# Performance work log

Hardware: AMD Instinct MI355X
Metric: run time of the kernel (lower is better)

Reference implementation:

```python
import jax, jax.numpy as jnp
import numpy as np

B, S, D, H, W = 4, 2048, 512, 8, 16
DK = D // H


def setup_inputs() -> dict:
    key = jax.random.key(0)
    ks = jax.random.split(key, 11)
    scale = 1.0 / np.sqrt(D)
    return {
        "query": jax.random.normal(ks[0], (B, S, D), jnp.float32),
        "key": jax.random.normal(ks[1], (B, S, D), jnp.float32),
        "value": jax.random.normal(ks[2], (B, S, D), jnp.float32),
        "Wq": jax.random.normal(ks[3], (D, D), jnp.float32) * scale,
        "bq": jnp.zeros((D,), jnp.float32),
        "Wk": jax.random.normal(ks[4], (D, D), jnp.float32) * scale,
        "bk": jnp.zeros((D,), jnp.float32),
        "Wv": jax.random.normal(ks[5], (D, D), jnp.float32) * scale,
        "bv": jnp.zeros((D,), jnp.float32),
        "Wo": jax.random.normal(ks[6], (D, D), jnp.float32) * scale,
        "bo": jnp.zeros((D,), jnp.float32),
    }


def reference(query, key, value, Wq, bq, Wk, bk, Wv, bv, Wo, bo):
    b, s, d = query.shape
    # QKV projections -> [b, H, s, DK]
    Q = (query @ Wq + bq).reshape(b, s, H, DK).transpose(0, 2, 1, 3)
    K = (key @ Wk + bk).reshape(b, s, H, DK).transpose(0, 2, 1, 3)
    V = (value @ Wv + bv).reshape(b, s, H, DK).transpose(0, 2, 1, 3)
    # Dense scores (faithful to original O(n^2) math), then static band mask
    scores = jnp.einsum("bhqd,bhkd->bhqk", Q, K) / jnp.sqrt(jnp.array(DK, scores_dtype := Q.dtype))
    idx = jnp.arange(s)
    local = jnp.abs(idx[:, None] - idx[None, :]) <= W  # [s, s] band
    mask_value = jnp.finfo(scores.dtype).min
    scores = jnp.where(local[None, None], scores, mask_value)
    attn = jax.nn.softmax(scores, axis=-1)
    ctx = jnp.einsum("bhqk,bhkd->bhqd", attn, V)
    ctx = ctx.transpose(0, 2, 1, 3).reshape(b, s, d)
    return ctx @ Wo + bo
```

## Files before the change

### kernel.cpp

```cpp
#include <hip/hip_runtime.h>

typedef __attribute__((ext_vector_type(8))) short bf16x8;
typedef __attribute__((ext_vector_type(4))) float f32x4;
typedef __attribute__((ext_vector_type(4))) unsigned int u32x4;
typedef __attribute__((ext_vector_type(8))) unsigned short bfu8;

#define BB 4
#define SS 2048
#define DD 512
#define HH 8
#define DKK 64
#define WWIN 16
#define MTOT (BB*SS)
#define MKE  ((long)MTOT*DD)
#define NKE  ((long)DD*DD)

__device__ __forceinline__ unsigned short f2bf(float f) {
  unsigned int u = __float_as_uint(f);
  u += 0x7fffu + ((u >> 16) & 1u);
  return (unsigned short)(u >> 16);
}
__device__ __forceinline__ float bf2f(unsigned short s) {
  return __uint_as_float(((unsigned int)s) << 16);
}

__device__ __forceinline__ void gload_lds16(const unsigned short* g, unsigned short* l) {
  __builtin_amdgcn_global_load_lds((const __attribute__((address_space(1))) void*)g,
                                   (__attribute__((address_space(3))) void*)l, 16, 0, 0);
}

__global__ __launch_bounds__(256) void convert_w(
    const float* __restrict__ Wq, const float* __restrict__ Wk,
    const float* __restrict__ Wv, const float* __restrict__ Wo,
    const float* __restrict__ bq, const float* __restrict__ bk, const float* __restrict__ bv,
    unsigned short* __restrict__ wt, float* __restrict__ bias_all)
{
  int bx = blockIdx.x;
  if (bx >= 256) {
    int idx = (bx - 256) * 256 + threadIdx.x;
    bias_all[idx] = idx < DD ? bq[idx] : (idx < 2*DD ? bk[idx-DD] : bv[idx-2*DD]);
    return;
  }
  int wm = bx >> 6;
  int tile = bx & 63;
  int tr = tile >> 3, tc = tile & 7;
  const float* src = wm==0 ? Wq : wm==1 ? Wk : wm==2 ? Wv : Wo;
  unsigned short* dst = wt + (long)wm*NKE;
  __shared__ float tl[64][65];
  int t = threadIdx.x;
  int cr = t >> 6;
  int cc = t & 63;
  for (int p = 0; p < 16; ++p) {
    int row = p*4 + cr;
    tl[row][cc] = src[(long)(tr*64+row)*DD + tc*64 + cc];
  }
  __syncthreads();
  for (int p = 0; p < 16; ++p) {
    int orow = p*4 + cr;
    dst[(long)(tc*64 + orow)*DD + tr*64 + cc] = f2bf(tl[cc][orow]);
  }
}

template<int OUT_BF16, int A_FP32>
__global__ __launch_bounds__(256, 2) void gemm_dbuf(
    const void* __restrict__ a0, const void* __restrict__ a1, const void* __restrict__ a2,
    const unsigned short* __restrict__ Btbase, long bZ,
    const float* __restrict__ biasBase, long biasZ,
    void* __restrict__ outBase, long outZ, int N, int K)
{
  const int bid   = blockIdx.x;
  const int slot  = bid >> 3;
  const int panel = (bid & 7) + 8 * (slot >> 2);
  const int n0 = (slot & 3) * 128;
  const int z  = panel >> 6;
  const int m0 = (panel & 63) * 128;

  const void* Av = z==0 ? a0 : z==1 ? a1 : a2;
  const unsigned short* Bt = Btbase + (long)z*bZ;
  const float* bias = biasBase + (long)z*biasZ;

  const int tid = threadIdx.x, lane = tid & 63, w = tid >> 6;
  const int wr = w >> 1, wc = w & 1;
  const int c = lane & 15, g = lane >> 4;

  __shared__ unsigned short lA[2][128*64];
  __shared__ unsigned short lB[2][128*64];

  f32x4 acc[4][4] = {};
  float4 fa[8];
  const int NT = K >> 6;

  auto stageB = [&](int buf, int kt) {
    #pragma unroll
    for (int j = 0; j < 4; ++j) {
      int u = w*256 + j*64 + lane;
      int row = u >> 3, sl = (u & 7) ^ (row & 7);
      gload_lds16(Bt + (long)(n0 + row)*K + kt + sl*8, &lB[buf][(w*256 + j*64)*8]);
    }
  };
  auto stageA_lds = [&](int buf, int kt) {
    const unsigned short* Ab = (const unsigned short*)Av;
    #pragma unroll
    for (int j = 0; j < 4; ++j) {
      int u = w*256 + j*64 + lane;
      int row = u >> 3, sl = (u & 7) ^ (row & 7);
      gload_lds16(Ab + (long)(m0 + row)*K + kt + sl*8, &lA[buf][(w*256 + j*64)*8]);
    }
  };
  auto loadA = [&](int kt) {
    const float* Af = (const float*)Av;
    #pragma unroll
    for (int i = 0; i < 4; ++i) {
      int u = i*256 + tid;
      int row = u >> 3, col = (u & 7) * 8;
      const float* s = Af + (long)(m0 + row)*K + kt + col;
      fa[2*i]   = *(const float4*)s;
      fa[2*i+1] = *(const float4*)(s + 4);
    }
  };
  auto writeA = [&](int buf) {
    #pragma unroll
    for (int i = 0; i < 4; ++i) {
      int u = i*256 + tid;
      int row = u >> 3, sl = u & 7;
      bfu8 o;
      o[0]=f2bf(fa[2*i].x);   o[1]=f2bf(fa[2*i].y);   o[2]=f2bf(fa[2*i].z);   o[3]=f2bf(fa[2*i].w);
      o[4]=f2bf(fa[2*i+1].x); o[5]=f2bf(fa[2*i+1].y); o[6]=f2bf(fa[2*i+1].z); o[7]=f2bf(fa[2*i+1].w);
      *(bfu8*)&lA[buf][row*64 + (sl ^ (row & 7))*8] = o;
    }
  };
  auto compute = [&](int buf) {
    #pragma unroll
    for (int kk = 0; kk < 2; ++kk) {
      bf16x8 af[4], bfr[4];
      #pragma unroll
      for (int m = 0; m < 4; ++m) {
        int row = wr*64 + m*16 + c;
        af[m] = *reinterpret_cast<const bf16x8*>(&lA[buf][row*64 + (((kk<<2)+g) ^ (row & 7))*8]);
      }
      #pragma unroll
      for (int nn = 0; nn < 4; ++nn) {
        int col = wc*64 + nn*16 + c;
        bfr[nn] = *reinterpret_cast<const bf16x8*>(&lB[buf][col*64 + (((kk<<2)+g) ^ (col & 7))*8]);
      }
      __builtin_amdgcn_s_setprio(1);
      #pragma unroll
      for (int m = 0; m < 4; ++m)
        #pragma unroll
        for (int nn = 0; nn < 4; ++nn)
          acc[m][nn] = __builtin_amdgcn_mfma_f32_16x16x32_bf16(af[m], bfr[nn], acc[m][nn], 0, 0, 0);
      __builtin_amdgcn_s_setprio(0);
    }
  };

  if (A_FP32) loadA(0); else stageA_lds(0, 0);
  stageB(0, 0);
  if (A_FP32) writeA(0);
  __syncthreads();

  int cur = 0;
  for (int t = 0; t < NT; ++t) {
    int nxt = cur ^ 1;
    if (t + 1 < NT) {
      if (A_FP32) loadA((t+1) << 6); else stageA_lds(nxt, (t+1) << 6);
      stageB(nxt, (t+1) << 6);
    }
    compute(cur);
    if (A_FP32 && t + 1 < NT) writeA(nxt);
    __syncthreads();
    cur = nxt;
  }

  #pragma unroll
  for (int m = 0; m < 4; ++m) {
    int rbase = m0 + wr*64 + m*16 + g*4;
    #pragma unroll
    for (int nn = 0; nn < 4; ++nn) {
      int col = n0 + wc*64 + nn*16 + c;
      float bv = bias[col];
      #pragma unroll
      for (int r = 0; r < 4; ++r) {
        float val = acc[m][nn][r] + bv;
        long idx = (long)z*outZ + (long)(rbase + r)*N + col;
        if (OUT_BF16) ((unsigned short*)outBase)[idx] = f2bf(val);
        else          ((float*)outBase)[idx] = val;
      }
    }
  }
}

#define KP 76
#define PP 76
__global__ __launch_bounds__(256) void attn_kernel(
    const unsigned short* __restrict__ Qbf, const unsigned short* __restrict__ Kbf,
    const unsigned short* __restrict__ Vbf, unsigned short* __restrict__ ctxbf)
{
  const int q0 = blockIdx.x * 128;
  const int h  = blockIdx.y;
  const int b  = blockIdx.z;
  const int tid = threadIdx.x, lane = tid & 63, w = tid >> 6;
  const int c = lane & 15, g = lane >> 4;
  const int w0 = q0 - WWIN;

  __shared__ unsigned short K_l[160*KP];
  __shared__ unsigned short V_l[160*KP];
  __shared__ unsigned short P_l[4][32*PP];

  const long baseRow = (long)b*SS*DD + (long)h*DKK;
  const int qw0   = q0 + w*32;
  const int kbase = w*32;

  bf16x8 aq[2][2];
  for (int m = 0; m < 2; ++m)
    for (int kk = 0; kk < 2; ++kk)
      aq[m][kk] = *reinterpret_cast<const bf16x8*>(
          Qbf + baseRow + (long)(qw0 + m*16 + c)*DD + kk*32 + g*8);

  for (int i = 0; i < 5; ++i) {
    int u = i*256 + tid;
    int row = u >> 3, c8 = (u & 7) * 8;
    int gk = w0 + row;
    u32x4 kv = {0,0,0,0}, vv = {0,0,0,0};
    if (gk >= 0 && gk < SS) {
      kv = *(const u32x4*)(Kbf + baseRow + (long)gk*DD + c8);
      vv = *(const u32x4*)(Vbf + baseRow + (long)gk*DD + c8);
    }
    *(u32x4*)(&K_l[row*KP + c8]) = kv;
    *(u32x4*)(&V_l[row*KP + c8]) = vv;
  }
  __syncthreads();

  f32x4 accs[2][4] = {};
  __builtin_amdgcn_s_setprio(1);
  for (int kk = 0; kk < 2; ++kk) {
    bf16x8 bk[4];
    for (int n = 0; n < 4; ++n)
      bk[n] = *reinterpret_cast<const bf16x8*>(&K_l[(kbase + n*16 + c)*KP + kk*32 + g*8]);
    for (int m = 0; m < 2; ++m)
      for (int n = 0; n < 4; ++n)
        accs[m][n] = __builtin_amdgcn_mfma_f32_16x16x32_bf16(aq[m][kk], bk[n], accs[m][n], 0, 0, 0);
  }
  __builtin_amdgcn_s_setprio(0);

  float pden[2][4];
  for (int m = 0; m < 2; ++m) {
    for (int r = 0; r < 4; ++r) {
      int qi = m*16 + g*4 + r;
      float sv[4];
      float mx = -INFINITY;
      for (int n = 0; n < 4; ++n) {
        int kr = n*16 + c;
        int d  = kr - qi;
        int kg = w0 + kbase + kr;
        bool ok = (d >= 0) && (d <= 2*WWIN) && (kg >= 0) && (kg < SS);
        sv[n] = ok ? accs[m][n][r] * 0.125f : -INFINITY;
        mx = fmaxf(mx, sv[n]);
      }
      for (int off = 1; off < 16; off <<= 1) mx = fmaxf(mx, __shfl_xor(mx, off, 64));
      float sum = 0.f;
      for (int n = 0; n < 4; ++n) {
        float e = __expf(sv[n] - mx);
        sum += e;
        P_l[w][(m*16 + g*4 + r)*PP + n*16 + c] = f2bf(e);
      }
      for (int off = 1; off < 16; off <<= 1) sum += __shfl_xor(sum, off, 64);
      pden[m][r] = sum;
    }
  }
  __syncthreads();

  f32x4 acco[2][4] = {};
  for (int kk = 0; kk < 2; ++kk) {
    bf16x8 pa[2];
    for (int m = 0; m < 2; ++m)
      pa[m] = *reinterpret_cast<const bf16x8*>(&P_l[w][(m*16 + c)*PP + kk*32 + g*8]);
    bf16x8 bv[4];
    int kb = kbase + kk*32 + g*8;
    for (int n = 0; n < 4; ++n) {
      bfu8 t;
      for (int j = 0; j < 8; ++j) t[j] = V_l[(kb + j)*KP + n*16 + c];
      bv[n] = *reinterpret_cast<bf16x8*>(&t);
    }
    __builtin_amdgcn_s_setprio(1);
    for (int m = 0; m < 2; ++m)
      for (int n = 0; n < 4; ++n)
        acco[m][n] = __builtin_amdgcn_mfma_f32_16x16x32_bf16(pa[m], bv[n], acco[m][n], 0, 0, 0);
    __builtin_amdgcn_s_setprio(0);
  }

  for (int m = 0; m < 2; ++m) {
    for (int r = 0; r < 4; ++r) {
      int q = qw0 + m*16 + g*4 + r;
      float inv = 1.f / pden[m][r];
      for (int n = 0; n < 4; ++n)
        ctxbf[baseRow + (long)q*DD + n*16 + c] = f2bf(acco[m][n][r] * inv);
    }
  }
}

extern "C" void kernel_launch(void* const* d_in, const int* in_sizes, int n_in,
                              void* d_out, int out_size, void* d_ws, size_t ws_size,
                              hipStream_t stream) {
  const float* q  = (const float*)d_in[0];
  const float* k  = (const float*)d_in[1];
  const float* v  = (const float*)d_in[2];
  const float* Wq = (const float*)d_in[3];
  const float* bq = (const float*)d_in[4];
  const float* Wk = (const float*)d_in[5];
  const float* bk = (const float*)d_in[6];
  const float* Wv = (const float*)d_in[7];
  const float* bv = (const float*)d_in[8];
  const float* Wo = (const float*)d_in[9];
  const float* bo = (const float*)d_in[10];

  char* ws = (char*)d_ws;
  unsigned short* wtbf     = (unsigned short*)(ws);
  float*          bias_all = (float*)(ws + 2097152);
  unsigned short* qkvbf    = (unsigned short*)(ws + 2103296);
  unsigned short* ctxbf    = (unsigned short*)(ws + 27269120);

  convert_w<<<262, 256, 0, stream>>>(Wq, Wk, Wv, Wo, bq, bk, bv, wtbf, bias_all);
  gemm_dbuf<1,1><<<768, 256, 0, stream>>>(
      q, k, v, wtbf, NKE, bias_all, DD,
      (void*)qkvbf, MKE, DD, DD);
  attn_kernel<<<dim3(SS/128, HH, BB), 256, 0, stream>>>(
      qkvbf, qkvbf + MKE, qkvbf + 2*MKE, ctxbf);
  gemm_dbuf<0,0><<<256, 256, 0, stream>>>(
      ctxbf, ctxbf, ctxbf, wtbf + 3*NKE, 0, bo, 0,
      (void*)d_out, 0, DD, DD);
}
```

Before: 158.4 us.

## Replace LDS double buffering with register-staged single-buffer GEMM pipeline

The GEMM kernel drops direct global-to-LDS loads and double-buffered shared memory. It now prefetches the next A and B tiles into registers while computing on a single LDS buffer, then writes them to LDS between explicit barriers. Halving LDS use allows raising the occupancy hint from 2 to 3 blocks per CU. The cost is two barriers per iteration and more register pressure, and the bf16 A path loses the async LDS load.

Result: no change. 156.6 us (-1.2%).

```diff
diff --git a/kernel.cpp b/kernel.cpp
--- a/kernel.cpp
+++ b/kernel.cpp
@@ -24,10 +24,10 @@
   return __uint_as_float(((unsigned int)s) << 16);
 }
 
-__device__ __forceinline__ void gload_lds16(const unsigned short* g, unsigned short* l) {
-  __builtin_amdgcn_global_load_lds((const __attribute__((address_space(1))) void*)g,
-                                   (__attribute__((address_space(3))) void*)l, 16, 0, 0);
-}
+#define SBAR() do { __builtin_amdgcn_sched_barrier(0); __builtin_amdgcn_s_barrier(); \
+                    __builtin_amdgcn_sched_barrier(0); } while (0)
+#define LGKM0() do { asm volatile("s_waitcnt lgkmcnt(0)" ::: "memory"); \
+                     __builtin_amdgcn_sched_barrier(0); } while (0)
 
 __global__ __launch_bounds__(256) void convert_w(
     const float* __restrict__ Wq, const float* __restrict__ Wk,
@@ -62,7 +62,7 @@
 }
 
 template<int OUT_BF16, int A_FP32>
-__global__ __launch_bounds__(256, 2) void gemm_dbuf(
+__global__ __launch_bounds__(256, 3) void gemm_pipe(
     const void* __restrict__ a0, const void* __restrict__ a1, const void* __restrict__ a2,
     const unsigned short* __restrict__ Btbase, long bZ,
     const float* __restrict__ biasBase, long biasZ,
@@ -83,65 +83,75 @@
   const int wr = w >> 1, wc = w & 1;
   const int c = lane & 15, g = lane >> 4;
 
-  __shared__ unsigned short lA[2][128*64];
-  __shared__ unsigned short lB[2][128*64];
+  __shared__ unsigned short lA[128*64];
+  __shared__ unsigned short lB[128*64];
 
   f32x4 acc[4][4] = {};
-  float4 fa[8];
+  float4 fa32[8];
+  bfu8   fa16[4];
+  bfu8   fb[4];
   const int NT = K >> 6;
 
-  auto stageB = [&](int buf, int kt) {
-    #pragma unroll
-    for (int j = 0; j < 4; ++j) {
-      int u = w*256 + j*64 + lane;
-      int row = u >> 3, sl = (u & 7) ^ (row & 7);
-      gload_lds16(Bt + (long)(n0 + row)*K + kt + sl*8, &lB[buf][(w*256 + j*64)*8]);
-    }
-  };
-  auto stageA_lds = [&](int buf, int kt) {
-    const unsigned short* Ab = (const unsigned short*)Av;
-    #pragma unroll
-    for (int j = 0; j < 4; ++j) {
-      int u = w*256 + j*64 + lane;
-      int row = u >> 3, sl = (u & 7) ^ (row & 7);
-      gload_lds16(Ab + (long)(m0 + row)*K + kt + sl*8, &lA[buf][(w*256 + j*64)*8]);
-    }
-  };
   auto loadA = [&](int kt) {
-    const float* Af = (const float*)Av;
+    if (A_FP32) {
+      const float* Af = (const float*)Av;
+      #pragma unroll
+      for (int i = 0; i < 4; ++i) {
+        int u = i*256 + tid, row = u >> 3, col = (u & 7) * 8;
+        const float* s = Af + (long)(m0 + row)*K + kt + col;
+        fa32[2*i]   = *(const float4*)s;
+        fa32[2*i+1] = *(const float4*)(s + 4);
+      }
+    } else {
+      const unsigned short* Ab = (const unsigned short*)Av;
+      #pragma unroll
+      for (int i = 0; i < 4; ++i) {
+        int u = i*256 + tid, row = u >> 3, col = (u & 7) * 8;
+        fa16[i] = *(const bfu8*)(Ab + (long)(m0 + row)*K + kt + col);
+      }
+    }
+  };
+  auto loadB = [&](int kt) {
     #pragma unroll
     for (int i = 0; i < 4; ++i) {
-      int u = i*256 + tid;
-      int row = u >> 3, col = (u & 7) * 8;
-      const float* s = Af + (long)(m0 + row)*K + kt + col;
-      fa[2*i]   = *(const float4*)s;
-      fa[2*i+1] = *(const float4*)(s + 4);
-    }
-  };
-  auto writeA = [&](int buf) {
+      int u = i*256 + tid, row = u >> 3, col = (u & 7) * 8;
+      fb[i] = *(const bfu8*)(Bt + (long)(n0 + row)*K + kt + col);
+    }
+  };
+  auto writeA = [&]() {
     #pragma unroll
     for (int i = 0; i < 4; ++i) {
-      int u = i*256 + tid;
-      int row = u >> 3, sl = u & 7;
+      int u = i*256 + tid, row = u >> 3, sl = u & 7;
       bfu8 o;
-      o[0]=f2bf(fa[2*i].x);   o[1]=f2bf(fa[2*i].y);   o[2]=f2bf(fa[2*i].z);   o[3]=f2bf(fa[2*i].w);
-      o[4]=f2bf(fa[2*i+1].x); o[5]=f2bf(fa[2*i+1].y); o[6]=f2bf(fa[2*i+1].z); o[7]=f2bf(fa[2*i+1].w);
-      *(bfu8*)&lA[buf][row*64 + (sl ^ (row & 7))*8] = o;
-    }
-  };
-  auto compute = [&](int buf) {
+      if (A_FP32) {
+        o[0]=f2bf(fa32[2*i].x);   o[1]=f2bf(fa32[2*i].y);
+        o[2]=f2bf(fa32[2*i].z);   o[3]=f2bf(fa32[2*i].w);
+        o[4]=f2bf(fa32[2*i+1].x); o[5]=f2bf(fa32[2*i+1].y);
+        o[6]=f2bf(fa32[2*i+1].z); o[7]=f2bf(fa32[2*i+1].w);
+      } else o = fa16[i];
+      *(bfu8*)&lA[row*64 + (sl ^ (row & 7))*8] = o;
+    }
+  };
+  auto writeB = [&]() {
+    #pragma unroll
+    for (int i = 0; i < 4; ++i) {
+      int u = i*256 + tid, row = u >> 3, sl = u & 7;
+      *(bfu8*)&lB[row*64 + (sl ^ (row & 7))*8] = fb[i];
+    }
+  };
+  auto compute = [&]() {
     #pragma unroll
     for (int kk = 0; kk < 2; ++kk) {
       bf16x8 af[4], bfr[4];
       #pragma unroll
       for (int m = 0; m < 4; ++m) {
         int row = wr*64 + m*16 + c;
-        af[m] = *reinterpret_cast<const bf16x8*>(&lA[buf][row*64 + (((kk<<2)+g) ^ (row & 7))*8]);
+        af[m] = *reinterpret_cast<const bf16x8*>(&lA[row*64 + (((kk<<2)+g) ^ (row & 7))*8]);
       }
       #pragma unroll
       for (int nn = 0; nn < 4; ++nn) {
         int col = wc*64 + nn*16 + c;
-        bfr[nn] = *reinterpret_cast<const bf16x8*>(&lB[buf][col*64 + (((kk<<2)+g) ^ (col & 7))*8]);
+        bfr[nn] = *reinterpret_cast<const bf16x8*>(&lB[col*64 + (((kk<<2)+g) ^ (col & 7))*8]);
       }
       __builtin_amdgcn_s_setprio(1);
       #pragma unroll
@@ -153,22 +163,18 @@
     }
   };
 
-  if (A_FP32) loadA(0); else stageA_lds(0, 0);
-  stageB(0, 0);
-  if (A_FP32) writeA(0);
-  __syncthreads();
-
-  int cur = 0;
+  loadA(0); loadB(0);
+  writeA(); writeB();
+  LGKM0(); SBAR();
+
   for (int t = 0; t < NT; ++t) {
-    int nxt = cur ^ 1;
+    if (t + 1 < NT) { loadA((t+1) << 6); loadB((t+1) << 6); }
+    compute();
     if (t + 1 < NT) {
-      if (A_FP32) loadA((t+1) << 6); else stageA_lds(nxt, (t+1) << 6);
-      stageB(nxt, (t+1) << 6);
-    }
-    compute(cur);
-    if (A_FP32 && t + 1 < NT) writeA(nxt);
-    __syncthreads();
-    cur = nxt;
+      SBAR();
+      writeA(); writeB();
+      LGKM0(); SBAR();
+    }
   }
 
   #pragma unroll
@@ -320,12 +326,12 @@
   unsigned short* ctxbf    = (unsigned short*)(ws + 27269120);
 
   convert_w<<<262, 256, 0, stream>>>(Wq, Wk, Wv, Wo, bq, bk, bv, wtbf, bias_all);
-  gemm_dbuf<1,1><<<768, 256, 0, stream>>>(
+  gemm_pipe<1,1><<<768, 256, 0, stream>>>(
       q, k, v, wtbf, NKE, bias_all, DD,
       (void*)qkvbf, MKE, DD, DD);
   attn_kernel<<<dim3(SS/128, HH, BB), 256, 0, stream>>>(
       qkvbf, qkvbf + MKE, qkvbf + 2*MKE, ctxbf);
-  gemm_dbuf<0,0><<<256, 256, 0, stream>>>(
+  gemm_pipe<0,0><<<256, 256, 0, stream>>>(
       ctxbf, ctxbf, ctxbf, wtbf + 3*NKE, 0, bo, 0,
       (void*)d_out, 0, DD, DD);
 }
```
